# Optimization experiments

Measured on AMD Instinct MI355X. Metric: run time of the kernel, lower is better.

The kernel has to match this reference:

```python
import jax, jax.numpy as jnp
import numpy as np

N_NODES = 50000


def _sage_conv(x, src, dst, W_l, W_r, b, num_nodes):
    # message = x[src]; scatter-mean onto dst (PyG SAGEConv aggr='mean')
    msg = x[src]                                                # [E, C_in]
    agg_sum = jax.ops.segment_sum(msg, dst, num_segments=num_nodes)
    deg = jax.ops.segment_sum(jnp.ones((src.shape[0],), x.dtype), dst,
                              num_segments=num_nodes)
    agg = agg_sum / jnp.maximum(deg, 1.0)[:, None]              # mean, deg clamped to 1
    # lin_l(agg) + lin_r(x); bias lives in lin_l (PyG default)
    return agg @ W_l.T + x @ W_r.T + b


def setup_inputs() -> dict:
    key = jax.random.key(0)
    ks = jax.random.split(key, 8)
    C = 128
    s = 1.0 / np.sqrt(C)
    x = jax.random.normal(ks[0], (N_NODES, C), dtype=jnp.float32)
    edge_index = jax.random.randint(ks[1], (2, 800000), 0, N_NODES, dtype=jnp.int64)
    W1_l = jax.random.uniform(ks[2], (C, C), jnp.float32, -s, s)
    W1_r = jax.random.uniform(ks[3], (C, C), jnp.float32, -s, s)
    b1 = jax.random.uniform(ks[4], (C,), jnp.float32, -s, s)
    W2_l = jax.random.uniform(ks[5], (C, C), jnp.float32, -s, s)
    W2_r = jax.random.uniform(ks[6], (C, C), jnp.float32, -s, s)
    b2 = jax.random.uniform(ks[7], (C,), jnp.float32, -s, s)
    return {"x": x, "edge_index": edge_index,
            "W1_l": W1_l, "W1_r": W1_r, "b1": b1,
            "W2_l": W2_l, "W2_r": W2_r, "b2": b2}


def reference(x, edge_index, W1_l, W1_r, b1, W2_l, W2_r, b2):
    src, dst = edge_index[0], edge_index[1]
    h = _sage_conv(x, src, dst, W1_l, W1_r, b1, N_NODES)
    h = jax.nn.relu(h)  # dropout p=0.0 -> no-op
    out = _sage_conv(h, src, dst, W2_l, W2_r, b2, N_NODES)
    return out
```

## Files before the change

### kernel.cpp

```cpp
#include <hip/hip_runtime.h>

#define NCH 128
#define MAXBKT 512
#define BKT_SHIFT 7
#define BKT_NODES 128
#define BIN_BATCH 4096
#define NHIST 128

typedef __attribute__((ext_vector_type(8))) short bf16x8;
typedef __attribute__((ext_vector_type(4))) float f32x4;

__device__ __forceinline__ unsigned short f2bf_rne(float f) {
  unsigned u = __float_as_uint(f);
  unsigned r = u + 0x7FFF + ((u >> 16) & 1);
  return (unsigned short)(r >> 16);
}

__global__ __launch_bounds__(256) void k_bkthist(const int* __restrict__ dst,
                                                 int* __restrict__ partial,
                                                 int nE, int nBkt) {
  __shared__ int h[MAXBKT];
  int t = threadIdx.x;
  h[t] = 0; h[t + 256] = 0;
  __syncthreads();
  for (int e = blockIdx.x * 256 + t; e < nE; e += gridDim.x * 256)
    atomicAdd(&h[dst[e] >> BKT_SHIFT], 1);
  __syncthreads();
  partial[blockIdx.x * MAXBKT + t] = h[t];
  partial[blockIdx.x * MAXBKT + t + 256] = h[t + 256];
}

__global__ __launch_bounds__(512) void k_bktscan(const int* __restrict__ partial,
                                                 int* __restrict__ bktBase,
                                                 int* __restrict__ bktCursor, int nBkt) {
  __shared__ int sc[512];
  int t = threadIdx.x;
  int v = 0;
#pragma unroll 8
  for (int b = 0; b < NHIST; b++) v += partial[b * MAXBKT + t];
  sc[t] = v;
  __syncthreads();
  for (int off = 1; off < 512; off <<= 1) {
    int u = (t >= off) ? sc[t - off] : 0;
    __syncthreads();
    sc[t] += u;
    __syncthreads();
  }
  bktBase[t] = sc[t] - v;
  if (t == 511) bktBase[512] = sc[511];
  bktCursor[t] = 0;
}

__global__ __launch_bounds__(256) void k_bin(const int* __restrict__ src,
                                             const int* __restrict__ dst,
                                             const int* __restrict__ bktBase,
                                             int* __restrict__ bktCursor,
                                             uint2* __restrict__ binned,
                                             int nE, int nBkt) {
  __shared__ int hist[MAXBKT];
  __shared__ int boff[MAXBKT];
  int t = threadIdx.x;
  hist[t] = 0; hist[t + 256] = 0;
  __syncthreads();

  int eb = blockIdx.x * BIN_BATCH;
  uint2 pr[16];
  int rk[16];
#pragma unroll
  for (int i = 0; i < 16; i++) {
    int e = eb + t + i * 256;
    if (e < nE) {
      pr[i] = make_uint2((unsigned)src[e], (unsigned)dst[e]);
      rk[i] = atomicAdd(&hist[pr[i].y >> BKT_SHIFT], 1);
    } else rk[i] = -1;
  }
  __syncthreads();
  for (int i = t; i < nBkt; i += 256)
    boff[i] = hist[i] ? atomicAdd(&bktCursor[i], hist[i]) : 0;
  __syncthreads();
#pragma unroll
  for (int i = 0; i < 16; i++) {
    if (rk[i] >= 0) {
      int b = pr[i].y >> BKT_SHIFT;
      binned[bktBase[b] + boff[b] + rk[i]] = pr[i];
    }
  }
}

__global__ __launch_bounds__(256) void k_build(const uint2* __restrict__ binned,
                                               const int* __restrict__ bktBase,
                                               int* __restrict__ start,
                                               float* __restrict__ invdeg,
                                               int* __restrict__ srcSorted,
                                               int nN, int nE) {
  __shared__ int cnt[BKT_NODES];
  __shared__ int sc[BKT_NODES];
  __shared__ int cur[BKT_NODES];
  int b = blockIdx.x, t = threadIdx.x;
  int base = b << BKT_SHIFT;
  int e0 = bktBase[b], e1 = bktBase[b + 1];

  if (t < BKT_NODES) { cnt[t] = 0; cur[t] = 0; }
  __syncthreads();
  for (int i = e0 + t; i < e1; i += 256)
    atomicAdd(&cnt[binned[i].y - base], 1);
  __syncthreads();
  if (t < BKT_NODES) sc[t] = cnt[t];
  __syncthreads();
  for (int off = 1; off < BKT_NODES; off <<= 1) {
    int u = (t < BKT_NODES && t >= off) ? sc[t - off] : 0;
    __syncthreads();
    if (t < BKT_NODES && t >= off) sc[t] += u;
    __syncthreads();
  }
  if (t < BKT_NODES) {
    int n = base + t;
    if (n < nN) {
      start[n] = e0 + sc[t] - cnt[t];
      invdeg[n] = 1.0f / fmaxf((float)cnt[t], 1.0f);
    }
  }
  if (b == 0 && t == 0) start[nN] = nE;
  __syncthreads();
  for (int i = e0 + t; i < e1; i += 256) {
    uint2 p = binned[i];
    int ld = p.y - base;
    int pos = e0 + sc[ld] - cnt[ld] + atomicAdd(&cur[ld], 1);
    srcSorted[pos] = (int)p.x;
  }
}

__device__ __forceinline__ void prepW_elem(const float* __restrict__ Wl,
                                           const float* __restrict__ Wr,
                                           unsigned short* __restrict__ WhiF,
                                           unsigned short* __restrict__ WloF, int i) {
  int kc   = i >> 12;
  int r    = i & 4095;
  int nt   = r >> 9;
  int r2   = r & 511;
  int lane = r2 >> 3;
  int e    = r2 & 7;
  int j = nt * 16 + (lane & 15);
  int k = kc * 32 + (lane >> 4) * 8 + e;
  float w = (k < 128) ? Wl[j * 128 + k] : Wr[j * 128 + (k - 128)];
  unsigned u = __float_as_uint(w);
  float fhi = __uint_as_float(u & 0xFFFF0000u);
  float flo = w - fhi;
  WhiF[i] = (unsigned short)(u >> 16);
  WloF[i] = (unsigned short)(__float_as_uint(flo) >> 16);
}

__global__ __launch_bounds__(256) void k_prep(const float* __restrict__ x,
                                              unsigned short* __restrict__ xbf,
                                              const float* __restrict__ W1l,
                                              const float* __restrict__ W1r,
                                              const float* __restrict__ W2l,
                                              const float* __restrict__ W2r,
                                              unsigned short* __restrict__ W1hi,
                                              unsigned short* __restrict__ W1lo,
                                              unsigned short* __restrict__ W2hi,
                                              unsigned short* __restrict__ W2lo,
                                              int n8) {
  int i = blockIdx.x * 256 + threadIdx.x;
  if (i < n8) {
    const float4* p = reinterpret_cast<const float4*>(x + (size_t)i * 8);
    float4 v0 = p[0], v1 = p[1];
    uint4 o;
    o.x = (unsigned)f2bf_rne(v0.x) | ((unsigned)f2bf_rne(v0.y) << 16);
    o.y = (unsigned)f2bf_rne(v0.z) | ((unsigned)f2bf_rne(v0.w) << 16);
    o.z = (unsigned)f2bf_rne(v1.x) | ((unsigned)f2bf_rne(v1.y) << 16);
    o.w = (unsigned)f2bf_rne(v1.z) | ((unsigned)f2bf_rne(v1.w) << 16);
    *reinterpret_cast<uint4*>(xbf + (size_t)i * 8) = o;
  } else {
    int j = i - n8;
    if (j < 32768)       prepW_elem(W1l, W1r, W1hi, W1lo, j);
    else if (j < 65536)  prepW_elem(W2l, W2r, W2hi, W2lo, j - 32768);
  }
}

#define ACC8(v)                                          \
  a0 += __uint_as_float((v).x << 16);                    \
  a1 += __uint_as_float((v).x & 0xFFFF0000u);            \
  a2 += __uint_as_float((v).y << 16);                    \
  a3 += __uint_as_float((v).y & 0xFFFF0000u);            \
  a4 += __uint_as_float((v).z << 16);                    \
  a5 += __uint_as_float((v).z & 0xFFFF0000u);            \
  a6 += __uint_as_float((v).w << 16);                    \
  a7 += __uint_as_float((v).w & 0xFFFF0000u);

__global__ __launch_bounds__(256) void k_gather(const unsigned short* __restrict__ xbf,
                                                const int* __restrict__ srcSorted,
                                                const int* __restrict__ start,
                                                const float* __restrict__ invdeg,
                                                unsigned short* __restrict__ aggbf,
                                                int nN) {
  int gid = blockIdx.x * 256 + threadIdx.x;
  int node = gid >> 4;
  if (node >= nN) return;
  int c = (gid & 15) << 3;
  const unsigned short* xb = xbf + c;
  int s0 = start[node], s1 = start[node + 1];
  float a0 = 0.f, a1 = 0.f, a2 = 0.f, a3 = 0.f,
        a4 = 0.f, a5 = 0.f, a6 = 0.f, a7 = 0.f;
  int i = s0;
  for (; i + 4 <= s1; i += 4) {
    int sa = srcSorted[i],      sb = srcSorted[i + 1];
    int sc_ = srcSorted[i + 2], sd = srcSorted[i + 3];
    uint4 va = *reinterpret_cast<const uint4*>(xb + (size_t)sa * NCH);
    uint4 vb = *reinterpret_cast<const uint4*>(xb + (size_t)sb * NCH);
    uint4 vc = *reinterpret_cast<const uint4*>(xb + (size_t)sc_ * NCH);
    uint4 vd = *reinterpret_cast<const uint4*>(xb + (size_t)sd * NCH);
    ACC8(va) ACC8(vb) ACC8(vc) ACC8(vd)
  }
  for (; i < s1; i++) {
    int s = srcSorted[i];
    uint4 v = *reinterpret_cast<const uint4*>(xb + (size_t)s * NCH);
    ACC8(v)
  }
  float idg = invdeg[node];
  uint4 o;
  o.x = (unsigned)f2bf_rne(a0 * idg) | ((unsigned)f2bf_rne(a1 * idg) << 16);
  o.y = (unsigned)f2bf_rne(a2 * idg) | ((unsigned)f2bf_rne(a3 * idg) << 16);
  o.z = (unsigned)f2bf_rne(a4 * idg) | ((unsigned)f2bf_rne(a5 * idg) << 16);
  o.w = (unsigned)f2bf_rne(a6 * idg) | ((unsigned)f2bf_rne(a7 * idg) << 16);
  *reinterpret_cast<uint4*>(aggbf + (size_t)node * NCH + c) = o;
}

__global__ __launch_bounds__(256, 4) void k_linear_mfma(
    const unsigned short* __restrict__ aggbf, const unsigned short* __restrict__ xinbf,
    const unsigned short* __restrict__ Whi, const unsigned short* __restrict__ Wlo,
    const float* __restrict__ bias, float* __restrict__ outF,
    unsigned short* __restrict__ outBf, int relu, int nNodes) {
  int t = threadIdx.x;
  int wave = t >> 6;
  int lane = t & 63;
  int l15 = lane & 15;
  int lq  = lane >> 4;
  int r0 = (blockIdx.x * 4 + wave) * 16;

  const bf16x8* WhiV = reinterpret_cast<const bf16x8*>(Whi) + lane;
  const bf16x8* WloV = reinterpret_cast<const bf16x8*>(Wlo) + lane;

  f32x4 acc[8];
#pragma unroll
  for (int i = 0; i < 8; i++) acc[i] = (f32x4){0.f, 0.f, 0.f, 0.f};

  int arow = r0 + l15;
  if (arow >= nNodes) arow = nNodes - 1;

#pragma unroll
  for (int kc = 0; kc < 8; kc++) {
    const unsigned short* ab = (kc < 4) ? aggbf : xinbf;
    int k128 = (kc & 3) * 32 + lq * 8;
    bf16x8 a = *reinterpret_cast<const bf16x8*>(ab + (size_t)arow * NCH + k128);
#pragma unroll
    for (int nt = 0; nt < 8; nt++) {
      int fidx = (kc * 8 + nt) * 64;
      bf16x8 bhi = WhiV[fidx];
      bf16x8 blo = WloV[fidx];
      acc[nt] = __builtin_amdgcn_mfma_f32_16x16x32_bf16(a, bhi, acc[nt], 0, 0, 0);
      acc[nt] = __builtin_amdgcn_mfma_f32_16x16x32_bf16(a, blo, acc[nt], 0, 0, 0);
    }
  }

#pragma unroll
  for (int nt = 0; nt < 8; nt++) {
    int col = nt * 16 + l15;
    float bv = bias[col];
#pragma unroll
    for (int i = 0; i < 4; i++) {
      int row = r0 + lq * 4 + i;
      if (row < nNodes) {
        float v = acc[nt][i] + bv;
        if (relu) v = fmaxf(v, 0.f);
        if (outBf) outBf[(size_t)row * NCH + col] = f2bf_rne(v);
        else       outF[(size_t)row * NCH + col] = v;
      }
    }
  }
}

extern "C" void kernel_launch(void* const* d_in, const int* in_sizes, int n_in,
                              void* d_out, int out_size, void* d_ws, size_t ws_size,
                              hipStream_t stream) {
  const float* x   = (const float*)d_in[0];
  const int*   ei  = (const int*)d_in[1];
  const float* W1l = (const float*)d_in[2];
  const float* W1r = (const float*)d_in[3];
  const float* b1  = (const float*)d_in[4];
  const float* W2l = (const float*)d_in[5];
  const float* W2r = (const float*)d_in[6];
  const float* b2  = (const float*)d_in[7];
  float* out = (float*)d_out;

  const int nE = in_sizes[1] / 2;
  const int nN = in_sizes[0] / NCH;
  const int* src = ei;
  const int* dst = ei + nE;
  const int nBkt = (nN + BKT_NODES - 1) >> BKT_SHIFT;

  size_t bfBytes = (size_t)nN * NCH * sizeof(unsigned short);
  size_t wBytes  = (size_t)128 * 256 * sizeof(unsigned short);
  auto align256 = [](size_t v) { return (v + 255) & ~(size_t)255; };

  char* ws = (char*)d_ws;
  unsigned short* xbf   = (unsigned short*)ws;  ws += bfBytes;
  unsigned short* aggbf = (unsigned short*)ws;  ws += bfBytes;
  unsigned short* hbf   = (unsigned short*)ws;  ws += bfBytes;
  uint2* binned    = (uint2*)ws;                ws += (size_t)nE * sizeof(uint2);
  int*   srcSorted = (int*)ws;                  ws += align256((size_t)nE * sizeof(int));
  int*   startRow  = (int*)ws;                  ws += align256((size_t)(nN + 1) * sizeof(int));
  float* invdeg    = (float*)ws;                ws += align256((size_t)nN * sizeof(float));
  int*   partial   = (int*)ws;                  ws += (size_t)NHIST * MAXBKT * sizeof(int);
  int*   bktCursor = (int*)ws;                  ws += MAXBKT * sizeof(int);
  int*   bktBase   = (int*)ws;                  ws += align256((MAXBKT + 1) * sizeof(int));
  unsigned short* W1hi = (unsigned short*)ws;   ws += wBytes;
  unsigned short* W1lo = (unsigned short*)ws;   ws += wBytes;
  unsigned short* W2hi = (unsigned short*)ws;   ws += wBytes;
  unsigned short* W2lo = (unsigned short*)ws;   ws += wBytes;

  k_bkthist<<<NHIST, 256, 0, stream>>>(dst, partial, nE, nBkt);
  k_bktscan<<<1, 512, 0, stream>>>(partial, bktBase, bktCursor, nBkt);
  k_bin<<<(nE + BIN_BATCH - 1) / BIN_BATCH, 256, 0, stream>>>(src, dst, bktBase,
                                                              bktCursor, binned, nE, nBkt);
  k_build<<<nBkt, 256, 0, stream>>>(binned, bktBase, startRow, invdeg, srcSorted, nN, nE);

  {
    int n8 = nN * NCH / 8;
    int total = n8 + 2 * 32768;
    k_prep<<<(total + 255) / 256, 256, 0, stream>>>(x, xbf, W1l, W1r, W2l, W2r,
                                                    W1hi, W1lo, W2hi, W2lo, n8);
  }

  int gatherBlocks = (nN * 16 + 255) / 256;
  int linBlocks = (nN + 63) / 64;

  k_gather<<<gatherBlocks, 256, 0, stream>>>(xbf, srcSorted, startRow, invdeg, aggbf, nN);
  k_linear_mfma<<<linBlocks, 256, 0, stream>>>(aggbf, xbf, W1hi, W1lo, b1,
                                               nullptr, hbf, 1, nN);

  k_gather<<<gatherBlocks, 256, 0, stream>>>(hbf, srcSorted, startRow, invdeg, aggbf, nN);
  k_linear_mfma<<<linBlocks, 256, 0, stream>>>(aggbf, hbf, W2hi, W2lo, b2,
                                               out, nullptr, 0, nN);
}
```

Before: 158.8 us.

## Fuse histogram with prep, pack binned edges, widen gather and linear tiles

The edge-histogram kernel and the x/W bf16 prep kernel are merged into one launch, and the partial-histogram layout is transposed so the scan can read it with int4 loads. Binned edges are packed into 32 bits (16-bit src plus local dst), which halves binning traffic but assumes fewer than 65536 nodes. Gather now uses a full wave per node: four sub-units split the edge list and are combined with shuffle reductions, exposing more memory-level parallelism. The MFMA linear kernel computes 32 rows per wave with launch bounds lowered to 3 waves per SIMD, and the bin batch and histogram block counts are retuned.

```diff
diff --git a/kernel.cpp b/kernel.cpp
--- a/kernel.cpp
+++ b/kernel.cpp
@@ -4,8 +4,8 @@
 #define MAXBKT 512
 #define BKT_SHIFT 7
 #define BKT_NODES 128
-#define BIN_BATCH 4096
-#define NHIST 128
+#define BIN_BATCH 1024
+#define NHIST 64
 
 typedef __attribute__((ext_vector_type(8))) short bf16x8;
 typedef __attribute__((ext_vector_type(4))) float f32x4;
@@ -14,120 +14,6 @@
   unsigned u = __float_as_uint(f);
   unsigned r = u + 0x7FFF + ((u >> 16) & 1);
   return (unsigned short)(r >> 16);
-}
-
-__global__ __launch_bounds__(256) void k_bkthist(const int* __restrict__ dst,
-                                                 int* __restrict__ partial,
-                                                 int nE, int nBkt) {
-  __shared__ int h[MAXBKT];
-  int t = threadIdx.x;
-  h[t] = 0; h[t + 256] = 0;
-  __syncthreads();
-  for (int e = blockIdx.x * 256 + t; e < nE; e += gridDim.x * 256)
-    atomicAdd(&h[dst[e] >> BKT_SHIFT], 1);
-  __syncthreads();
-  partial[blockIdx.x * MAXBKT + t] = h[t];
-  partial[blockIdx.x * MAXBKT + t + 256] = h[t + 256];
-}
-
-__global__ __launch_bounds__(512) void k_bktscan(const int* __restrict__ partial,
-                                                 int* __restrict__ bktBase,
-                                                 int* __restrict__ bktCursor, int nBkt) {
-  __shared__ int sc[512];
-  int t = threadIdx.x;
-  int v = 0;
-#pragma unroll 8
-  for (int b = 0; b < NHIST; b++) v += partial[b * MAXBKT + t];
-  sc[t] = v;
-  __syncthreads();
-  for (int off = 1; off < 512; off <<= 1) {
-    int u = (t >= off) ? sc[t - off] : 0;
-    __syncthreads();
-    sc[t] += u;
-    __syncthreads();
-  }
-  bktBase[t] = sc[t] - v;
-  if (t == 511) bktBase[512] = sc[511];
-  bktCursor[t] = 0;
-}
-
-__global__ __launch_bounds__(256) void k_bin(const int* __restrict__ src,
-                                             const int* __restrict__ dst,
-                                             const int* __restrict__ bktBase,
-                                             int* __restrict__ bktCursor,
-                                             uint2* __restrict__ binned,
-                                             int nE, int nBkt) {
-  __shared__ int hist[MAXBKT];
-  __shared__ int boff[MAXBKT];
-  int t = threadIdx.x;
-  hist[t] = 0; hist[t + 256] = 0;
-  __syncthreads();
-
-  int eb = blockIdx.x * BIN_BATCH;
-  uint2 pr[16];
-  int rk[16];
-#pragma unroll
-  for (int i = 0; i < 16; i++) {
-    int e = eb + t + i * 256;
-    if (e < nE) {
-      pr[i] = make_uint2((unsigned)src[e], (unsigned)dst[e]);
-      rk[i] = atomicAdd(&hist[pr[i].y >> BKT_SHIFT], 1);
-    } else rk[i] = -1;
-  }
-  __syncthreads();
-  for (int i = t; i < nBkt; i += 256)
-    boff[i] = hist[i] ? atomicAdd(&bktCursor[i], hist[i]) : 0;
-  __syncthreads();
-#pragma unroll
-  for (int i = 0; i < 16; i++) {
-    if (rk[i] >= 0) {
-      int b = pr[i].y >> BKT_SHIFT;
-      binned[bktBase[b] + boff[b] + rk[i]] = pr[i];
-    }
-  }
-}
-
-__global__ __launch_bounds__(256) void k_build(const uint2* __restrict__ binned,
-                                               const int* __restrict__ bktBase,
-                                               int* __restrict__ start,
-                                               float* __restrict__ invdeg,
-                                               int* __restrict__ srcSorted,
-                                               int nN, int nE) {
-  __shared__ int cnt[BKT_NODES];
-  __shared__ int sc[BKT_NODES];
-  __shared__ int cur[BKT_NODES];
-  int b = blockIdx.x, t = threadIdx.x;
-  int base = b << BKT_SHIFT;
-  int e0 = bktBase[b], e1 = bktBase[b + 1];
-
-  if (t < BKT_NODES) { cnt[t] = 0; cur[t] = 0; }
-  __syncthreads();
-  for (int i = e0 + t; i < e1; i += 256)
-    atomicAdd(&cnt[binned[i].y - base], 1);
-  __syncthreads();
-  if (t < BKT_NODES) sc[t] = cnt[t];
-  __syncthreads();
-  for (int off = 1; off < BKT_NODES; off <<= 1) {
-    int u = (t < BKT_NODES && t >= off) ? sc[t - off] : 0;
-    __syncthreads();
-    if (t < BKT_NODES && t >= off) sc[t] += u;
-    __syncthreads();
-  }
-  if (t < BKT_NODES) {
-    int n = base + t;
-    if (n < nN) {
-      start[n] = e0 + sc[t] - cnt[t];
-      invdeg[n] = 1.0f / fmaxf((float)cnt[t], 1.0f);
-    }
-  }
-  if (b == 0 && t == 0) start[nN] = nE;
-  __syncthreads();
-  for (int i = e0 + t; i < e1; i += 256) {
-    uint2 p = binned[i];
-    int ld = p.y - base;
-    int pos = e0 + sc[ld] - cnt[ld] + atomicAdd(&cur[ld], 1);
-    srcSorted[pos] = (int)p.x;
-  }
 }
 
 __device__ __forceinline__ void prepW_elem(const float* __restrict__ Wl,
@@ -150,31 +36,147 @@
   WloF[i] = (unsigned short)(__float_as_uint(flo) >> 16);
 }
 
-__global__ __launch_bounds__(256) void k_prep(const float* __restrict__ x,
-                                              unsigned short* __restrict__ xbf,
-                                              const float* __restrict__ W1l,
-                                              const float* __restrict__ W1r,
-                                              const float* __restrict__ W2l,
-                                              const float* __restrict__ W2r,
-                                              unsigned short* __restrict__ W1hi,
-                                              unsigned short* __restrict__ W1lo,
-                                              unsigned short* __restrict__ W2hi,
-                                              unsigned short* __restrict__ W2lo,
-                                              int n8) {
-  int i = blockIdx.x * 256 + threadIdx.x;
-  if (i < n8) {
-    const float4* p = reinterpret_cast<const float4*>(x + (size_t)i * 8);
-    float4 v0 = p[0], v1 = p[1];
-    uint4 o;
-    o.x = (unsigned)f2bf_rne(v0.x) | ((unsigned)f2bf_rne(v0.y) << 16);
-    o.y = (unsigned)f2bf_rne(v0.z) | ((unsigned)f2bf_rne(v0.w) << 16);
-    o.z = (unsigned)f2bf_rne(v1.x) | ((unsigned)f2bf_rne(v1.y) << 16);
-    o.w = (unsigned)f2bf_rne(v1.z) | ((unsigned)f2bf_rne(v1.w) << 16);
-    *reinterpret_cast<uint4*>(xbf + (size_t)i * 8) = o;
+__global__ __launch_bounds__(256) void k_hist_prep(
+    const int* __restrict__ dst, int* __restrict__ partial,
+    const float* __restrict__ x, unsigned short* __restrict__ xbf,
+    const float* __restrict__ W1l, const float* __restrict__ W1r,
+    const float* __restrict__ W2l, const float* __restrict__ W2r,
+    unsigned short* __restrict__ W1hi, unsigned short* __restrict__ W1lo,
+    unsigned short* __restrict__ W2hi, unsigned short* __restrict__ W2lo,
+    int nE, int n8) {
+  int t = threadIdx.x;
+  if (blockIdx.x < NHIST) {
+    __shared__ int h[MAXBKT];
+    h[t] = 0; h[t + 256] = 0;
+    __syncthreads();
+    for (int e = blockIdx.x * 256 + t; e < nE; e += NHIST * 256)
+      atomicAdd(&h[dst[e] >> BKT_SHIFT], 1);
+    __syncthreads();
+    partial[t * NHIST + blockIdx.x] = h[t];
+    partial[(t + 256) * NHIST + blockIdx.x] = h[t + 256];
   } else {
-    int j = i - n8;
-    if (j < 32768)       prepW_elem(W1l, W1r, W1hi, W1lo, j);
-    else if (j < 65536)  prepW_elem(W2l, W2r, W2hi, W2lo, j - 32768);
+    int i = (blockIdx.x - NHIST) * 256 + t;
+    if (i < n8) {
+      const float4* p = reinterpret_cast<const float4*>(x + (size_t)i * 8);
+      float4 v0 = p[0], v1 = p[1];
+      uint4 o;
+      o.x = (unsigned)f2bf_rne(v0.x) | ((unsigned)f2bf_rne(v0.y) << 16);
+      o.y = (unsigned)f2bf_rne(v0.z) | ((unsigned)f2bf_rne(v0.w) << 16);
+      o.z = (unsigned)f2bf_rne(v1.x) | ((unsigned)f2bf_rne(v1.y) << 16);
+      o.w = (unsigned)f2bf_rne(v1.z) | ((unsigned)f2bf_rne(v1.w) << 16);
+      *reinterpret_cast<uint4*>(xbf + (size_t)i * 8) = o;
+    } else {
+      int j = i - n8;
+      if (j < 32768)       prepW_elem(W1l, W1r, W1hi, W1lo, j);
+      else if (j < 65536)  prepW_elem(W2l, W2r, W2hi, W2lo, j - 32768);
+    }
+  }
+}
+
+__global__ __launch_bounds__(512) void k_bktscan(const int* __restrict__ partial,
+                                                 int* __restrict__ bktBase,
+                                                 int* __restrict__ bktCursor, int nBkt) {
+  __shared__ int sc[512];
+  int t = threadIdx.x;
+  int v = 0;
+  const int4* p4 = reinterpret_cast<const int4*>(partial + t * NHIST);
+#pragma unroll
+  for (int b = 0; b < NHIST / 4; b++) {
+    int4 d = p4[b];
+    v += d.x + d.y + d.z + d.w;
+  }
+  sc[t] = v;
+  __syncthreads();
+  for (int off = 1; off < 512; off <<= 1) {
+    int u = (t >= off) ? sc[t - off] : 0;
+    __syncthreads();
+    sc[t] += u;
+    __syncthreads();
+  }
+  bktBase[t] = sc[t] - v;
+  if (t == 511) bktBase[512] = sc[511];
+  bktCursor[t] = 0;
+}
+
+__global__ __launch_bounds__(256) void k_bin(const int* __restrict__ src,
+                                             const int* __restrict__ dst,
+                                             const int* __restrict__ bktBase,
+                                             int* __restrict__ bktCursor,
+                                             unsigned* __restrict__ binned,
+                                             int nE, int nBkt) {
+  __shared__ int hist[MAXBKT];
+  __shared__ int boff[MAXBKT];
+  int t = threadIdx.x;
+  hist[t] = 0; hist[t + 256] = 0;
+  __syncthreads();
+
+  int eb = blockIdx.x * BIN_BATCH;
+  unsigned pk[4];
+  short bkt[4];
+  int rk[4];
+#pragma unroll
+  for (int i = 0; i < 4; i++) {
+    int e = eb + t + i * 256;
+    if (e < nE) {
+      int s = src[e], d = dst[e];
+      bkt[i] = (short)(d >> BKT_SHIFT);
+      pk[i] = (unsigned)s | ((unsigned)(d & (BKT_NODES - 1)) << 16);
+      rk[i] = atomicAdd(&hist[d >> BKT_SHIFT], 1);
+    } else rk[i] = -1;
+  }
+  __syncthreads();
+  for (int i = t; i < nBkt; i += 256)
+    boff[i] = hist[i] ? atomicAdd(&bktCursor[i], hist[i]) : 0;
+  __syncthreads();
+#pragma unroll
+  for (int i = 0; i < 4; i++) {
+    if (rk[i] >= 0) {
+      int b = bkt[i];
+      binned[bktBase[b] + boff[b] + rk[i]] = pk[i];
+    }
+  }
+}
+
+__global__ __launch_bounds__(256) void k_build(const unsigned* __restrict__ binned,
+                                               const int* __restrict__ bktBase,
+                                               int* __restrict__ start,
+                                               float* __restrict__ invdeg,
+                                               int* __restrict__ srcSorted,
+                                               int nN, int nE) {
+  __shared__ int cnt[BKT_NODES];
+  __shared__ int sc[BKT_NODES];
+  __shared__ int cur[BKT_NODES];
+  int b = blockIdx.x, t = threadIdx.x;
+  int base = b << BKT_SHIFT;
+  int e0 = bktBase[b], e1 = bktBase[b + 1];
+
+  if (t < BKT_NODES) { cnt[t] = 0; cur[t] = 0; }
+  __syncthreads();
+  for (int i = e0 + t; i < e1; i += 256)
+    atomicAdd(&cnt[binned[i] >> 16], 1);
+  __syncthreads();
+  if (t < BKT_NODES) sc[t] = cnt[t];
+  __syncthreads();
+  for (int off = 1; off < BKT_NODES; off <<= 1) {
+    int u = (t < BKT_NODES && t >= off) ? sc[t - off] : 0;
+    __syncthreads();
+    if (t < BKT_NODES && t >= off) sc[t] += u;
+    __syncthreads();
+  }
+  if (t < BKT_NODES) {
+    int n = base + t;
+    if (n < nN) {
+      start[n] = e0 + sc[t] - cnt[t];
+      invdeg[n] = 1.0f / fmaxf((float)cnt[t], 1.0f);
+    }
+  }
+  if (b == 0 && t == 0) start[nN] = nE;
+  __syncthreads();
+  for (int i = e0 + t; i < e1; i += 256) {
+    unsigned p = binned[i];
+    int ld = p >> 16;
+    int pos = e0 + sc[ld] - cnt[ld] + atomicAdd(&cur[ld], 1);
+    srcSorted[pos] = (int)(p & 0xFFFFu);
   }
 }
 
@@ -194,39 +196,52 @@
                                                 const float* __restrict__ invdeg,
                                                 unsigned short* __restrict__ aggbf,
                                                 int nN) {
-  int gid = blockIdx.x * 256 + threadIdx.x;
-  int node = gid >> 4;
+  int node = (blockIdx.x * 256 + threadIdx.x) >> 6;
   if (node >= nN) return;
-  int c = (gid & 15) << 3;
-  const unsigned short* xb = xbf + c;
+  int lane = threadIdx.x & 63;
+  int unit = lane >> 4;
+  int ul   = lane & 15;
+  const unsigned short* xb = xbf + ul * 8;
+
   int s0 = start[node], s1 = start[node + 1];
   float a0 = 0.f, a1 = 0.f, a2 = 0.f, a3 = 0.f,
         a4 = 0.f, a5 = 0.f, a6 = 0.f, a7 = 0.f;
-  int i = s0;
-  for (; i + 4 <= s1; i += 4) {
-    int sa = srcSorted[i],      sb = srcSorted[i + 1];
-    int sc_ = srcSorted[i + 2], sd = srcSorted[i + 3];
+  int i = s0 + unit;
+  for (; i + 12 < s1; i += 16) {
+    int sa = srcSorted[i],     sb = srcSorted[i + 4];
+    int sc = srcSorted[i + 8], sd = srcSorted[i + 12];
     uint4 va = *reinterpret_cast<const uint4*>(xb + (size_t)sa * NCH);
     uint4 vb = *reinterpret_cast<const uint4*>(xb + (size_t)sb * NCH);
-    uint4 vc = *reinterpret_cast<const uint4*>(xb + (size_t)sc_ * NCH);
+    uint4 vc = *reinterpret_cast<const uint4*>(xb + (size_t)sc * NCH);
     uint4 vd = *reinterpret_cast<const uint4*>(xb + (size_t)sd * NCH);
     ACC8(va) ACC8(vb) ACC8(vc) ACC8(vd)
   }
-  for (; i < s1; i++) {
+  for (; i < s1; i += 4) {
     int s = srcSorted[i];
     uint4 v = *reinterpret_cast<const uint4*>(xb + (size_t)s * NCH);
     ACC8(v)
   }
-  float idg = invdeg[node];
-  uint4 o;
-  o.x = (unsigned)f2bf_rne(a0 * idg) | ((unsigned)f2bf_rne(a1 * idg) << 16);
-  o.y = (unsigned)f2bf_rne(a2 * idg) | ((unsigned)f2bf_rne(a3 * idg) << 16);
-  o.z = (unsigned)f2bf_rne(a4 * idg) | ((unsigned)f2bf_rne(a5 * idg) << 16);
-  o.w = (unsigned)f2bf_rne(a6 * idg) | ((unsigned)f2bf_rne(a7 * idg) << 16);
-  *reinterpret_cast<uint4*>(aggbf + (size_t)node * NCH + c) = o;
-}
-
-__global__ __launch_bounds__(256, 4) void k_linear_mfma(
+  a0 += __shfl_xor(a0, 16); a0 += __shfl_xor(a0, 32);
+  a1 += __shfl_xor(a1, 16); a1 += __shfl_xor(a1, 32);
+  a2 += __shfl_xor(a2, 16); a2 += __shfl_xor(a2, 32);
+  a3 += __shfl_xor(a3, 16); a3 += __shfl_xor(a3, 32);
+  a4 += __shfl_xor(a4, 16); a4 += __shfl_xor(a4, 32);
+  a5 += __shfl_xor(a5, 16); a5 += __shfl_xor(a5, 32);
+  a6 += __shfl_xor(a6, 16); a6 += __shfl_xor(a6, 32);
+  a7 += __shfl_xor(a7, 16); a7 += __shfl_xor(a7, 32);
+
+  if (lane < 16) {
+    float idg = invdeg[node];
+    uint4 o;
+    o.x = (unsigned)f2bf_rne(a0 * idg) | ((unsigned)f2bf_rne(a1 * idg) << 16);
+    o.y = (unsigned)f2bf_rne(a2 * idg) | ((unsigned)f2bf_rne(a3 * idg) << 16);
+    o.z = (unsigned)f2bf_rne(a4 * idg) | ((unsigned)f2bf_rne(a5 * idg) << 16);
+    o.w = (unsigned)f2bf_rne(a6 * idg) | ((unsigned)f2bf_rne(a7 * idg) << 16);
+    *reinterpret_cast<uint4*>(aggbf + (size_t)node * NCH + ul * 8) = o;
+  }
+}
+
+__global__ __launch_bounds__(256, 3) void k_linear_mfma(
     const unsigned short* __restrict__ aggbf, const unsigned short* __restrict__ xinbf,
     const unsigned short* __restrict__ Whi, const unsigned short* __restrict__ Wlo,
     const float* __restrict__ bias, float* __restrict__ outF,
@@ -236,30 +251,36 @@
   int lane = t & 63;
   int l15 = lane & 15;
   int lq  = lane >> 4;
-  int r0 = (blockIdx.x * 4 + wave) * 16;
+  int r0 = (blockIdx.x * 4 + wave) * 32;
 
   const bf16x8* WhiV = reinterpret_cast<const bf16x8*>(Whi) + lane;
   const bf16x8* WloV = reinterpret_cast<const bf16x8*>(Wlo) + lane;
 
-  f32x4 acc[8];
-#pragma unroll
-  for (int i = 0; i < 8; i++) acc[i] = (f32x4){0.f, 0.f, 0.f, 0.f};
-
-  int arow = r0 + l15;
-  if (arow >= nNodes) arow = nNodes - 1;
+  f32x4 accA[8], accB[8];
+#pragma unroll
+  for (int i = 0; i < 8; i++) {
+    accA[i] = (f32x4){0.f, 0.f, 0.f, 0.f};
+    accB[i] = (f32x4){0.f, 0.f, 0.f, 0.f};
+  }
+
+  int rA = r0 + l15;        if (rA >= nNodes) rA = nNodes - 1;
+  int rB = r0 + 16 + l15;   if (rB >= nNodes) rB = nNodes - 1;
 
 #pragma unroll
   for (int kc = 0; kc < 8; kc++) {
     const unsigned short* ab = (kc < 4) ? aggbf : xinbf;
     int k128 = (kc & 3) * 32 + lq * 8;
-    bf16x8 a = *reinterpret_cast<const bf16x8*>(ab + (size_t)arow * NCH + k128);
+    bf16x8 aA = *reinterpret_cast<const bf16x8*>(ab + (size_t)rA * NCH + k128);
+    bf16x8 aB = *reinterpret_cast<const bf16x8*>(ab + (size_t)rB * NCH + k128);
 #pragma unroll
     for (int nt = 0; nt < 8; nt++) {
       int fidx = (kc * 8 + nt) * 64;
       bf16x8 bhi = WhiV[fidx];
       bf16x8 blo = WloV[fidx];
-      acc[nt] = __builtin_amdgcn_mfma_f32_16x16x32_bf16(a, bhi, acc[nt], 0, 0, 0);
-      acc[nt] = __builtin_amdgcn_mfma_f32_16x16x32_bf16(a, blo, acc[nt], 0, 0, 0);
+      accA[nt] = __builtin_amdgcn_mfma_f32_16x16x32_bf16(aA, bhi, accA[nt], 0, 0, 0);
+      accA[nt] = __builtin_amdgcn_mfma_f32_16x16x32_bf16(aA, blo, accA[nt], 0, 0, 0);
+      accB[nt] = __builtin_amdgcn_mfma_f32_16x16x32_bf16(aB, bhi, accB[nt], 0, 0, 0);
+      accB[nt] = __builtin_amdgcn_mfma_f32_16x16x32_bf16(aB, blo, accB[nt], 0, 0, 0);
     }
   }
 
@@ -269,12 +290,19 @@
     float bv = bias[col];
 #pragma unroll
     for (int i = 0; i < 4; i++) {
-      int row = r0 + lq * 4 + i;
-      if (row < nNodes) {
-        float v = acc[nt][i] + bv;
+      int rowA = r0 + lq * 4 + i;
+      if (rowA < nNodes) {
+        float v = accA[nt][i] + bv;
         if (relu) v = fmaxf(v, 0.f);
-        if (outBf) outBf[(size_t)row * NCH + col] = f2bf_rne(v);
-        else       outF[(size_t)row * NCH + col] = v;
+        if (outBf) outBf[(size_t)rowA * NCH + col] = f2bf_rne(v);
+        else       outF[(size_t)rowA * NCH + col] = v;
+      }
+      int rowB = r0 + 16 + lq * 4 + i;
+      if (rowB < nNodes) {
+        float v = accB[nt][i] + bv;
+        if (relu) v = fmaxf(v, 0.f);
+        if (outBf) outBf[(size_t)rowB * NCH + col] = f2bf_rne(v);
+        else       outF[(size_t)rowB * NCH + col] = v;
       }
     }
   }
@@ -307,7 +335,7 @@
   unsigned short* xbf   = (unsigned short*)ws;  ws += bfBytes;
   unsigned short* aggbf = (unsigned short*)ws;  ws += bfBytes;
   unsigned short* hbf   = (unsigned short*)ws;  ws += bfBytes;
-  uint2* binned    = (uint2*)ws;                ws += (size_t)nE * sizeof(uint2);
+  unsigned* binned = (unsigned*)ws;             ws += align256((size_t)nE * sizeof(unsigned));
   int*   srcSorted = (int*)ws;                  ws += align256((size_t)nE * sizeof(int));
   int*   startRow  = (int*)ws;                  ws += align256((size_t)(nN + 1) * sizeof(int));
   float* invdeg    = (float*)ws;                ws += align256((size_t)nN * sizeof(float));
@@ -319,21 +347,19 @@
   unsigned short* W2hi = (unsigned short*)ws;   ws += wBytes;
   unsigned short* W2lo = (unsigned short*)ws;   ws += wBytes;
 
-  k_bkthist<<<NHIST, 256, 0, stream>>>(dst, partial, nE, nBkt);
+  int n8 = nN * NCH / 8;
+  int prepBlocks = (n8 + 2 * 32768) / 256;
+
+  k_hist_prep<<<NHIST + prepBlocks, 256, 0, stream>>>(dst, partial, x, xbf,
+                                                      W1l, W1r, W2l, W2r,
+                                                      W1hi, W1lo, W2hi, W2lo, nE, n8);
   k_bktscan<<<1, 512, 0, stream>>>(partial, bktBase, bktCursor, nBkt);
   k_bin<<<(nE + BIN_BATCH - 1) / BIN_BATCH, 256, 0, stream>>>(src, dst, bktBase,
                                                               bktCursor, binned, nE, nBkt);
   k_build<<<nBkt, 256, 0, stream>>>(binned, bktBase, startRow, invdeg, srcSorted, nN, nE);
 
-  {
-    int n8 = nN * NCH / 8;
-    int total = n8 + 2 * 32768;
-    k_prep<<<(total + 255) / 256, 256, 0, stream>>>(x, xbf, W1l, W1r, W2l, W2r,
-                                                    W1hi, W1lo, W2hi, W2lo, n8);
-  }
-
-  int gatherBlocks = (nN * 16 + 255) / 256;
-  int linBlocks = (nN + 63) / 64;
+  int gatherBlocks = (nN * 64 + 255) / 256;
+  int linBlocks = (nN + 127) / 128;
 
   k_gather<<<gatherBlocks, 256, 0, stream>>>(xbf, srcSorted, startRow, invdeg, aggbf, nN);
   k_linear_mfma<<<linBlocks, 256, 0, stream>>>(aggbf, xbf, W1hi, W1lo, b1,
```

After: 184.6 us. +16.3%, slower.

## Pack binned edges to 32 bits, drop split-bf16 weights, unroll gather by 8

Applied to the files above, without the earlier changes.

Binned edges are packed into one 32-bit word, with the source in the low 16 bits and the local destination in the high bits. This halves the binning traffic. Weights are now rounded to a single bf16 copy instead of a hi/lo pair, which halves the MFMA count and weight loads in the linear kernel at some cost in accuracy. The gather loop adds an 8-way unrolled path for more memory-level parallelism, and the histogram stride becomes a compile-time constant. The 16-bit source field cannot hold node ids of 65536 or more, so correctness depends on the node count staying below that limit.

```diff
diff --git a/kernel.cpp b/kernel.cpp
--- a/kernel.cpp
+++ b/kernel.cpp
@@ -23,7 +23,7 @@
   int t = threadIdx.x;
   h[t] = 0; h[t + 256] = 0;
   __syncthreads();
-  for (int e = blockIdx.x * 256 + t; e < nE; e += gridDim.x * 256)
+  for (int e = blockIdx.x * 256 + t; e < nE; e += NHIST * 256)
     atomicAdd(&h[dst[e] >> BKT_SHIFT], 1);
   __syncthreads();
   partial[blockIdx.x * MAXBKT + t] = h[t];
@@ -55,7 +55,7 @@
                                              const int* __restrict__ dst,
                                              const int* __restrict__ bktBase,
                                              int* __restrict__ bktCursor,
-                                             uint2* __restrict__ binned,
+                                             unsigned* __restrict__ binned,
                                              int nE, int nBkt) {
   __shared__ int hist[MAXBKT];
   __shared__ int boff[MAXBKT];
@@ -64,14 +64,17 @@
   __syncthreads();
 
   int eb = blockIdx.x * BIN_BATCH;
-  uint2 pr[16];
+  unsigned pk[16];
+  short bkt[16];
   int rk[16];
 #pragma unroll
   for (int i = 0; i < 16; i++) {
     int e = eb + t + i * 256;
     if (e < nE) {
-      pr[i] = make_uint2((unsigned)src[e], (unsigned)dst[e]);
-      rk[i] = atomicAdd(&hist[pr[i].y >> BKT_SHIFT], 1);
+      int s = src[e], d = dst[e];
+      bkt[i] = (short)(d >> BKT_SHIFT);
+      pk[i] = (unsigned)s | ((unsigned)(d & (BKT_NODES - 1)) << 16);
+      rk[i] = atomicAdd(&hist[d >> BKT_SHIFT], 1);
     } else rk[i] = -1;
   }
   __syncthreads();
@@ -81,13 +84,13 @@
 #pragma unroll
   for (int i = 0; i < 16; i++) {
     if (rk[i] >= 0) {
-      int b = pr[i].y >> BKT_SHIFT;
-      binned[bktBase[b] + boff[b] + rk[i]] = pr[i];
+      int b = bkt[i];
+      binned[bktBase[b] + boff[b] + rk[i]] = pk[i];
     }
   }
 }
 
-__global__ __launch_bounds__(256) void k_build(const uint2* __restrict__ binned,
+__global__ __launch_bounds__(256) void k_build(const unsigned* __restrict__ binned,
                                                const int* __restrict__ bktBase,
                                                int* __restrict__ start,
                                                float* __restrict__ invdeg,
@@ -103,7 +106,7 @@
   if (t < BKT_NODES) { cnt[t] = 0; cur[t] = 0; }
   __syncthreads();
   for (int i = e0 + t; i < e1; i += 256)
-    atomicAdd(&cnt[binned[i].y - base], 1);
+    atomicAdd(&cnt[binned[i] >> 16], 1);
   __syncthreads();
   if (t < BKT_NODES) sc[t] = cnt[t];
   __syncthreads();
@@ -123,17 +126,16 @@
   if (b == 0 && t == 0) start[nN] = nE;
   __syncthreads();
   for (int i = e0 + t; i < e1; i += 256) {
-    uint2 p = binned[i];
-    int ld = p.y - base;
+    unsigned p = binned[i];
+    int ld = p >> 16;
     int pos = e0 + sc[ld] - cnt[ld] + atomicAdd(&cur[ld], 1);
-    srcSorted[pos] = (int)p.x;
+    srcSorted[pos] = (int)(p & 0xFFFFu);
   }
 }
 
 __device__ __forceinline__ void prepW_elem(const float* __restrict__ Wl,
                                            const float* __restrict__ Wr,
-                                           unsigned short* __restrict__ WhiF,
-                                           unsigned short* __restrict__ WloF, int i) {
+                                           unsigned short* __restrict__ WF, int i) {
   int kc   = i >> 12;
   int r    = i & 4095;
   int nt   = r >> 9;
@@ -143,11 +145,7 @@
   int j = nt * 16 + (lane & 15);
   int k = kc * 32 + (lane >> 4) * 8 + e;
   float w = (k < 128) ? Wl[j * 128 + k] : Wr[j * 128 + (k - 128)];
-  unsigned u = __float_as_uint(w);
-  float fhi = __uint_as_float(u & 0xFFFF0000u);
-  float flo = w - fhi;
-  WhiF[i] = (unsigned short)(u >> 16);
-  WloF[i] = (unsigned short)(__float_as_uint(flo) >> 16);
+  WF[i] = f2bf_rne(w);
 }
 
 __global__ __launch_bounds__(256) void k_prep(const float* __restrict__ x,
@@ -156,10 +154,8 @@
                                               const float* __restrict__ W1r,
                                               const float* __restrict__ W2l,
                                               const float* __restrict__ W2r,
-                                              unsigned short* __restrict__ W1hi,
-                                              unsigned short* __restrict__ W1lo,
-                                              unsigned short* __restrict__ W2hi,
-                                              unsigned short* __restrict__ W2lo,
+                                              unsigned short* __restrict__ W1f,
+                                              unsigned short* __restrict__ W2f,
                                               int n8) {
   int i = blockIdx.x * 256 + threadIdx.x;
   if (i < n8) {
@@ -173,8 +169,8 @@
     *reinterpret_cast<uint4*>(xbf + (size_t)i * 8) = o;
   } else {
     int j = i - n8;
-    if (j < 32768)       prepW_elem(W1l, W1r, W1hi, W1lo, j);
-    else if (j < 65536)  prepW_elem(W2l, W2r, W2hi, W2lo, j - 32768);
+    if (j < 32768)       prepW_elem(W1l, W1r, W1f, j);
+    else if (j < 65536)  prepW_elem(W2l, W2r, W2f, j - 32768);
   }
 }
 
@@ -203,14 +199,30 @@
   float a0 = 0.f, a1 = 0.f, a2 = 0.f, a3 = 0.f,
         a4 = 0.f, a5 = 0.f, a6 = 0.f, a7 = 0.f;
   int i = s0;
+  for (; i + 8 <= s1; i += 8) {
+    int s_0 = srcSorted[i],     s_1 = srcSorted[i + 1];
+    int s_2 = srcSorted[i + 2], s_3 = srcSorted[i + 3];
+    int s_4 = srcSorted[i + 4], s_5 = srcSorted[i + 5];
+    int s_6 = srcSorted[i + 6], s_7 = srcSorted[i + 7];
+    uint4 v0 = *reinterpret_cast<const uint4*>(xb + (size_t)s_0 * NCH);
+    uint4 v1 = *reinterpret_cast<const uint4*>(xb + (size_t)s_1 * NCH);
+    uint4 v2 = *reinterpret_cast<const uint4*>(xb + (size_t)s_2 * NCH);
+    uint4 v3 = *reinterpret_cast<const uint4*>(xb + (size_t)s_3 * NCH);
+    uint4 v4 = *reinterpret_cast<const uint4*>(xb + (size_t)s_4 * NCH);
+    uint4 v5 = *reinterpret_cast<const uint4*>(xb + (size_t)s_5 * NCH);
+    uint4 v6 = *reinterpret_cast<const uint4*>(xb + (size_t)s_6 * NCH);
+    uint4 v7 = *reinterpret_cast<const uint4*>(xb + (size_t)s_7 * NCH);
+    ACC8(v0) ACC8(v1) ACC8(v2) ACC8(v3)
+    ACC8(v4) ACC8(v5) ACC8(v6) ACC8(v7)
+  }
   for (; i + 4 <= s1; i += 4) {
-    int sa = srcSorted[i],      sb = srcSorted[i + 1];
-    int sc_ = srcSorted[i + 2], sd = srcSorted[i + 3];
-    uint4 va = *reinterpret_cast<const uint4*>(xb + (size_t)sa * NCH);
-    uint4 vb = *reinterpret_cast<const uint4*>(xb + (size_t)sb * NCH);
-    uint4 vc = *reinterpret_cast<const uint4*>(xb + (size_t)sc_ * NCH);
-    uint4 vd = *reinterpret_cast<const uint4*>(xb + (size_t)sd * NCH);
-    ACC8(va) ACC8(vb) ACC8(vc) ACC8(vd)
+    int s_0 = srcSorted[i],     s_1 = srcSorted[i + 1];
+    int s_2 = srcSorted[i + 2], s_3 = srcSorted[i + 3];
+    uint4 v0 = *reinterpret_cast<const uint4*>(xb + (size_t)s_0 * NCH);
+    uint4 v1 = *reinterpret_cast<const uint4*>(xb + (size_t)s_1 * NCH);
+    uint4 v2 = *reinterpret_cast<const uint4*>(xb + (size_t)s_2 * NCH);
+    uint4 v3 = *reinterpret_cast<const uint4*>(xb + (size_t)s_3 * NCH);
+    ACC8(v0) ACC8(v1) ACC8(v2) ACC8(v3)
   }
   for (; i < s1; i++) {
     int s = srcSorted[i];
@@ -228,7 +240,7 @@
 
 __global__ __launch_bounds__(256, 4) void k_linear_mfma(
     const unsigned short* __restrict__ aggbf, const unsigned short* __restrict__ xinbf,
-    const unsigned short* __restrict__ Whi, const unsigned short* __restrict__ Wlo,
+    const unsigned short* __restrict__ Wf,
     const float* __restrict__ bias, float* __restrict__ outF,
     unsigned short* __restrict__ outBf, int relu, int nNodes) {
   int t = threadIdx.x;
@@ -238,8 +250,7 @@
   int lq  = lane >> 4;
   int r0 = (blockIdx.x * 4 + wave) * 16;
 
-  const bf16x8* WhiV = reinterpret_cast<const bf16x8*>(Whi) + lane;
-  const bf16x8* WloV = reinterpret_cast<const bf16x8*>(Wlo) + lane;
+  const bf16x8* WV = reinterpret_cast<const bf16x8*>(Wf) + lane;
 
   f32x4 acc[8];
 #pragma unroll
@@ -255,11 +266,8 @@
     bf16x8 a = *reinterpret_cast<const bf16x8*>(ab + (size_t)arow * NCH + k128);
 #pragma unroll
     for (int nt = 0; nt < 8; nt++) {
-      int fidx = (kc * 8 + nt) * 64;
-      bf16x8 bhi = WhiV[fidx];
-      bf16x8 blo = WloV[fidx];
-      acc[nt] = __builtin_amdgcn_mfma_f32_16x16x32_bf16(a, bhi, acc[nt], 0, 0, 0);
-      acc[nt] = __builtin_amdgcn_mfma_f32_16x16x32_bf16(a, blo, acc[nt], 0, 0, 0);
+      bf16x8 bw = WV[(kc * 8 + nt) * 64];
+      acc[nt] = __builtin_amdgcn_mfma_f32_16x16x32_bf16(a, bw, acc[nt], 0, 0, 0);
     }
   }
 
@@ -307,17 +315,15 @@
   unsigned short* xbf   = (unsigned short*)ws;  ws += bfBytes;
   unsigned short* aggbf = (unsigned short*)ws;  ws += bfBytes;
   unsigned short* hbf   = (unsigned short*)ws;  ws += bfBytes;
-  uint2* binned    = (uint2*)ws;                ws += (size_t)nE * sizeof(uint2);
+  unsigned* binned = (unsigned*)ws;             ws += align256((size_t)nE * sizeof(unsigned));
   int*   srcSorted = (int*)ws;                  ws += align256((size_t)nE * sizeof(int));
   int*   startRow  = (int*)ws;                  ws += align256((size_t)(nN + 1) * sizeof(int));
   float* invdeg    = (float*)ws;                ws += align256((size_t)nN * sizeof(float));
   int*   partial   = (int*)ws;                  ws += (size_t)NHIST * MAXBKT * sizeof(int);
   int*   bktCursor = (int*)ws;                  ws += MAXBKT * sizeof(int);
   int*   bktBase   = (int*)ws;                  ws += align256((MAXBKT + 1) * sizeof(int));
-  unsigned short* W1hi = (unsigned short*)ws;   ws += wBytes;
-  unsigned short* W1lo = (unsigned short*)ws;   ws += wBytes;
-  unsigned short* W2hi = (unsigned short*)ws;   ws += wBytes;
-  unsigned short* W2lo = (unsigned short*)ws;   ws += wBytes;
+  unsigned short* W1f = (unsigned short*)ws;    ws += wBytes;
+  unsigned short* W2f = (unsigned short*)ws;    ws += wBytes;
 
   k_bkthist<<<NHIST, 256, 0, stream>>>(dst, partial, nE, nBkt);
   k_bktscan<<<1, 512, 0, stream>>>(partial, bktBase, bktCursor, nBkt);
@@ -329,17 +335,17 @@
     int n8 = nN * NCH / 8;
     int total = n8 + 2 * 32768;
     k_prep<<<(total + 255) / 256, 256, 0, stream>>>(x, xbf, W1l, W1r, W2l, W2r,
-                                                    W1hi, W1lo, W2hi, W2lo, n8);
+                                                    W1f, W2f, n8);
   }
 
   int gatherBlocks = (nN * 16 + 255) / 256;
   int linBlocks = (nN + 63) / 64;
 
   k_gather<<<gatherBlocks, 256, 0, stream>>>(xbf, srcSorted, startRow, invdeg, aggbf, nN);
-  k_linear_mfma<<<linBlocks, 256, 0, stream>>>(aggbf, xbf, W1hi, W1lo, b1,
+  k_linear_mfma<<<linBlocks, 256, 0, stream>>>(aggbf, xbf, W1f, b1,
                                                nullptr, hbf, 1, nN);
 
   k_gather<<<gatherBlocks, 256, 0, stream>>>(hbf, srcSorted, startRow, invdeg, aggbf, nN);
-  k_linear_mfma<<<linBlocks, 256, 0, stream>>>(aggbf, hbf, W2hi, W2lo, b2,
+  k_linear_mfma<<<linBlocks, 256, 0, stream>>>(aggbf, hbf, W2f, b2,
                                                out, nullptr, 0, nN);
 }
```

New measurement: 148.0 us (median of 2 runs). 6.8% less time.
